# Kernel optimization log

Measured on AMD Instinct MI355X. Metric: run time of the kernel, lower is better.

Reference implementation:

```python
import jax, jax.numpy as jnp
import numpy as np

NUM_TRUE = 8
NUM_NULL = 2
NUM_EXPERTS = NUM_TRUE + NUM_NULL
TOP_K = 2


def setup_inputs() -> dict:
    key = jax.random.key(0)
    k0, k1, k2 = jax.random.split(key, 3)
    B, S, D = 4, 2048, 1024
    inputs = jax.random.normal(k0, (B, S, D), dtype=jnp.float32)
    gate_w = jax.random.normal(k1, (NUM_EXPERTS, D), dtype=jnp.float32) * 0.02
    gate_b = jnp.zeros((NUM_EXPERTS,), dtype=jnp.float32)
    # expert_w stored as [E, D_in, D_out] so expert i computes x @ expert_w[i] + expert_b[i]
    expert_w = jax.random.normal(k2, (NUM_TRUE, D, D), dtype=jnp.float32) * 0.02
    expert_b = jnp.zeros((NUM_TRUE, D), dtype=jnp.float32)
    return {"inputs": inputs, "gate_w": gate_w, "gate_b": gate_b,
            "expert_w": expert_w, "expert_b": expert_b}


def reference(inputs, gate_w, gate_b, expert_w, expert_b):
    D = inputs.shape[-1]
    x = inputs.reshape(-1, D)                       # [T, D]
    gate_logits = x @ gate_w.T + gate_b             # [T, E]
    gate_probs = jax.nn.softmax(gate_logits, axis=-1)
    weights, selected = jax.lax.top_k(gate_probs, TOP_K)  # [T, K]
    true_mask = selected < NUM_TRUE                 # null experts contribute nothing
    true_weights = weights * true_mask
    denom = true_weights.sum(axis=-1, keepdims=True)
    denom = jnp.where(denom > 0, denom, jnp.ones_like(denom))
    norm_w = (true_weights / denom).astype(x.dtype)  # [T, K]
    # per-(token, true-expert) combine weight; zero for unselected experts
    one_hot = jax.nn.one_hot(selected, NUM_EXPERTS, dtype=norm_w.dtype)  # [T, K, E]
    combine_w = jnp.einsum('tk,tke->te', norm_w, one_hot)[:, :NUM_TRUE]  # [T, E_true]
    # dense expert evaluation, then weighted combine (zero weights cancel
    # exactly as the gather/scatter loop in the torch code)
    expert_out = jnp.einsum('td,edh->teh', x, expert_w) + expert_b[None, :, :]  # [T, E_true, D]
    out = jnp.einsum('te,teh->th', combine_w, expert_out)  # [T, D]
    return out.reshape(inputs.shape[:-1] + (out.shape[-1],))
```

## Files before the change

### kernel.cpp

```cpp
#include <hip/hip_runtime.h>
#include <hip/hip_bf16.h>
#include <stdint.h>

#define T_TOKENS 8192
#define D_DIM    1024
#define NE       10
#define NT       8
#define SEG      2048

typedef unsigned short u16;
typedef __attribute__((ext_vector_type(8))) __bf16 bf16x8;
typedef __attribute__((ext_vector_type(4))) float  f32x4;
typedef __attribute__((ext_vector_type(8))) unsigned short u16x8;
typedef __attribute__((ext_vector_type(4))) unsigned short u16x4;

static __device__ __forceinline__ u16 f32_to_bf16(float f) {
  union { float f; uint32_t u; } v; v.f = f;
  uint32_t u = v.u;
  return (u16)((u + 0x7fffu + ((u >> 16) & 1u)) >> 16);
}
static __device__ __forceinline__ float bf16_to_f32(u16 u) {
  union { uint32_t u; float f; } v; v.u = ((uint32_t)u) << 16; return v.f;
}

static __device__ __forceinline__ void async_load16(const u16* g, u16* l) {
  __builtin_amdgcn_global_load_lds(
      (const __attribute__((address_space(1))) void*)(const void*)g,
      (__attribute__((address_space(3))) void*)(void*)l, 16, 0, 0);
}

union PrepShared {
  struct { float gws[NE * D_DIM]; float gbs[NE]; int se[32]; float swt[32]; } g;
  struct { float tile[64][68]; } t;
};

__global__ __launch_bounds__(256) void prep_kernel(
    const float* __restrict__ x, const float* __restrict__ gw,
    const float* __restrict__ gb, const float* __restrict__ W,
    u16* __restrict__ xb, u16* __restrict__ wT,
    int* __restrict__ cnt, int* __restrict__ tokList,
    int* __restrict__ revIdx, float* __restrict__ revW) {
  __shared__ PrepShared sh;
  int tid = threadIdx.x;

  if (blockIdx.x >= 512) {
    int tb = blockIdx.x - 512;
    int e  = tb >> 8;
    int rem = tb & 255;
    int k0 = (rem >> 4) * 64;
    int n0 = (rem & 15) * 64;
    int cr = tid & 15;
    int r0 = tid >> 4;
    const float* We = W + ((size_t)e << 20);
#pragma unroll
    for (int pass = 0; pass < 4; ++pass) {
      int r = pass * 16 + r0;
      f32x4 v = *(const f32x4*)&We[(size_t)(k0 + r) * 1024 + n0 + cr * 4];
#pragma unroll
      for (int j = 0; j < 4; ++j) sh.t.tile[cr * 4 + j][r] = v[j];
    }
    __syncthreads();
    u16* wTe = wT + ((size_t)e << 20);
#pragma unroll
    for (int pass = 0; pass < 4; ++pass) {
      int n = pass * 16 + r0;
      f32x4 tv = *(const f32x4*)&sh.t.tile[n][cr * 4];
      u16x4 pk;
#pragma unroll
      for (int j = 0; j < 4; ++j) pk[j] = f32_to_bf16(tv[j]);
      *(u16x4*)&wTe[(size_t)(n0 + n) * 1024 + k0 + cr * 4] = pk;
    }
    return;
  }

  {
    const f32x4* g4 = (const f32x4*)gw;
    f32x4* s4 = (f32x4*)sh.g.gws;
    for (int i = tid; i < NE * D_DIM / 4; i += 256) s4[i] = g4[i];
  }
  if (tid < NE) sh.g.gbs[tid] = gb[tid];
  __syncthreads();
  int lane = tid & 63;
  int wv   = tid >> 6;
  const f32x4* gws4 = (const f32x4*)sh.g.gws;
  for (int it = 0; it < 4; ++it) {
    int slot = wv * 4 + it;
    int t = blockIdx.x * 16 + slot;
    const f32x4* xr4 = (const f32x4*)(x + (size_t)t * D_DIM);
    f32x4 xv[4];
#pragma unroll
    for (int jj = 0; jj < 4; ++jj) xv[jj] = xr4[lane + 64 * jj];
    u16x4* xbr = (u16x4*)(xb + (size_t)t * D_DIM);
#pragma unroll
    for (int jj = 0; jj < 4; ++jj) {
      u16x4 pk;
#pragma unroll
      for (int k = 0; k < 4; ++k) pk[k] = f32_to_bf16(xv[jj][k]);
      xbr[lane + 64 * jj] = pk;
    }
    float logit[NE];
#pragma unroll
    for (int e = 0; e < NE; ++e) {
      float a = 0.f;
#pragma unroll
      for (int jj = 0; jj < 4; ++jj) {
        f32x4 gv = gws4[e * 256 + lane + 64 * jj];
#pragma unroll
        for (int k = 0; k < 4; ++k) a = fmaf(xv[jj][k], gv[k], a);
      }
#pragma unroll
      for (int off = 32; off >= 1; off >>= 1) a += __shfl_xor(a, off);
      logit[e] = a + sh.g.gbs[e];
    }
    float mx = logit[0];
#pragma unroll
    for (int e = 1; e < NE; ++e) mx = fmaxf(mx, logit[e]);
    float p[NE]; float s = 0.f;
#pragma unroll
    for (int e = 0; e < NE; ++e) { p[e] = expf(logit[e] - mx); s += p[e]; }
    int e0 = 0; float b0 = p[0];
#pragma unroll
    for (int e = 1; e < NE; ++e) if (p[e] > b0) { b0 = p[e]; e0 = e; }
    int e1 = -1; float b1 = -1.f;
#pragma unroll
    for (int e = 0; e < NE; ++e) if (e != e0 && p[e] > b1) { b1 = p[e]; e1 = e; }
    float w0 = b0 / s, w1 = b1 / s;
    float tw0 = (e0 < NT) ? w0 : 0.f;
    float tw1 = (e1 < NT) ? w1 : 0.f;
    float denom = tw0 + tw1;
    float nw0 = 0.f, nw1 = 0.f;
    if (denom > 0.f) { nw0 = tw0 / denom; nw1 = tw1 / denom; }
    if (lane == 0) {
      sh.g.se[slot * 2]     = (e0 < NT) ? e0 : -1;  sh.g.swt[slot * 2]     = nw0;
      sh.g.se[slot * 2 + 1] = (e1 < NT) ? e1 : -1;  sh.g.swt[slot * 2 + 1] = nw1;
      if (e0 >= NT) { revIdx[t * 2]     = -1; revW[t * 2]     = 0.f; }
      if (e1 >= NT) { revIdx[t * 2 + 1] = -1; revW[t * 2 + 1] = 0.f; }
    }
  }
  __syncthreads();
  if (tid < NT) {
    int e = tid, c = 0;
    for (int i = 0; i < 32; ++i) c += (sh.g.se[i] == e);
    if (c > 0) {
      int base = atomicAdd(&cnt[e * 32], c);
      int j = 0;
      for (int i = 0; i < 32; ++i) {
        if (sh.g.se[i] == e) {
          int tt  = blockIdx.x * 16 + (i >> 1);
          int pos = base + j;
          tokList[e * SEG + pos]   = tt;
          revIdx[tt * 2 + (i & 1)] = e * SEG + pos;
          revW[tt * 2 + (i & 1)]   = sh.g.swt[i];
          ++j;
        }
      }
    }
  }
}

__global__ __launch_bounds__(512) void moe_gemm(
    const u16* __restrict__ xb, const u16* __restrict__ wT,
    const int* __restrict__ cnt, const int* __restrict__ tokList,
    const float* __restrict__ eb, u16* __restrict__ ybuf) {
  int e  = blockIdx.x;
  int c  = cnt[e * 32];
  int m0 = blockIdx.z * 128;
  if (m0 >= c) return;
  int n0 = blockIdx.y * 128;
  __shared__ __align__(16) u16 As[3][128 * 32];
  __shared__ __align__(16) u16 Bs[3][128 * 32];
  __shared__ int tokS[128];
  int tid = threadIdx.x;
  if (tid < 128) {
    int gm = m0 + tid;
    tokS[tid] = (gm < c) ? tokList[e * SEG + gm] : tokList[e * SEG];
  }
  __syncthreads();
  int lane = tid & 63;
  int wv   = tid >> 6;
  int rl  = lane >> 2;
  int kcp = lane & 3;
  int kcd = kcp ^ ((rl >> 1) & 3);
  int rowL = wv * 16 + rl;
  const u16* gA0 = xb + (size_t)tokS[rowL] * 1024 + kcd * 8;
  const u16* wTe = wT + ((size_t)e << 20);
  const u16* gB0 = wTe + (size_t)(n0 + rowL) * 1024 + kcd * 8;
  int ldsO = (wv * 16) * 32;

  int wm = wv >> 2, wn = wv & 3;
  int lrow = lane & 15;
  int q    = lane >> 4;
  int sw   = (q ^ ((lrow >> 1) & 3)) * 8;
  f32x4 acc[4][2];
#pragma unroll
  for (int i = 0; i < 4; ++i)
#pragma unroll
    for (int j = 0; j < 2; ++j) acc[i][j] = (f32x4){0.f, 0.f, 0.f, 0.f};

#pragma unroll
  for (int p = 0; p < 2; ++p) {
    int ko = p * 32;
    async_load16(gA0 + ko, As[p] + ldsO);
    async_load16(gB0 + ko, Bs[p] + ldsO);
  }

  int cur = 0;
  for (int kt = 0; kt < 32; ++kt) {
    asm volatile("s_barrier" ::: "memory");
    if (kt < 30) {
      int st = cur - 1; if (st < 0) st += 3;
      int ko = (kt + 2) * 32;
      async_load16(gA0 + ko, As[st] + ldsO);
      async_load16(gB0 + ko, Bs[st] + ldsO);
      asm volatile("s_waitcnt vmcnt(4)" ::: "memory");
    } else if (kt == 30) {
      asm volatile("s_waitcnt vmcnt(2)" ::: "memory");
    } else {
      asm volatile("s_waitcnt vmcnt(0)" ::: "memory");
    }
    asm volatile("s_barrier" ::: "memory");
    bf16x8 af[4], bfr[2];
#pragma unroll
    for (int mt = 0; mt < 4; ++mt)
      af[mt] = *(const bf16x8*)(As[cur] + (wm * 64 + mt * 16 + lrow) * 32 + sw);
#pragma unroll
    for (int nt = 0; nt < 2; ++nt)
      bfr[nt] = *(const bf16x8*)(Bs[cur] + (wn * 32 + nt * 16 + lrow) * 32 + sw);
#pragma unroll
    for (int mt = 0; mt < 4; ++mt)
#pragma unroll
      for (int nt = 0; nt < 2; ++nt)
        acc[mt][nt] = __builtin_amdgcn_mfma_f32_16x16x32_bf16(
            af[mt], bfr[nt], acc[mt][nt], 0, 0, 0);
    ++cur; if (cur == 3) cur = 0;
  }
  int rq = lane >> 4;
  float bias[2];
#pragma unroll
  for (int nt = 0; nt < 2; ++nt)
    bias[nt] = eb[e * 1024 + n0 + wn * 32 + nt * 16 + lrow];
  u16* yb = ybuf + ((size_t)(e * SEG + m0)) * 1024 + n0 + wn * 32 + lrow;
#pragma unroll
  for (int mt = 0; mt < 4; ++mt) {
#pragma unroll
    for (int r = 0; r < 4; ++r) {
      int ml = wm * 64 + mt * 16 + rq * 4 + r;
      u16* row = yb + (size_t)ml * 1024;
#pragma unroll
      for (int nt = 0; nt < 2; ++nt)
        row[nt * 16] = f32_to_bf16(acc[mt][nt][r] + bias[nt]);
    }
  }
}

__global__ __launch_bounds__(256) void combine_kernel(
    const u16* __restrict__ ybuf, const int* __restrict__ revIdx,
    const float* __restrict__ revW, float* __restrict__ out) {
  int tid = threadIdx.x, lane = tid & 63, wv = tid >> 6;
  for (int it = 0; it < 4; ++it) {
    int t  = blockIdx.x * 16 + wv * 4 + it;
    int i0 = revIdx[t * 2], i1 = revIdx[t * 2 + 1];
    float w0 = revW[t * 2], w1 = revW[t * 2 + 1];
    float o[16];
#pragma unroll
    for (int k = 0; k < 16; ++k) o[k] = 0.f;
    if (i0 >= 0) {
      const u16x8* y = (const u16x8*)(ybuf + (size_t)i0 * 1024);
#pragma unroll
      for (int jj = 0; jj < 2; ++jj) {
        u16x8 v = y[lane + 64 * jj];
#pragma unroll
        for (int k = 0; k < 8; ++k) o[jj * 8 + k] += w0 * bf16_to_f32(v[k]);
      }
    }
    if (i1 >= 0) {
      const u16x8* y = (const u16x8*)(ybuf + (size_t)i1 * 1024);
#pragma unroll
      for (int jj = 0; jj < 2; ++jj) {
        u16x8 v = y[lane + 64 * jj];
#pragma unroll
        for (int k = 0; k < 8; ++k) o[jj * 8 + k] += w1 * bf16_to_f32(v[k]);
      }
    }
    f32x4* o4 = (f32x4*)(out + (size_t)t * 1024);
#pragma unroll
    for (int jj = 0; jj < 2; ++jj)
#pragma unroll
      for (int h = 0; h < 2; ++h) {
        f32x4 vv = {o[jj * 8 + h * 4], o[jj * 8 + h * 4 + 1],
                    o[jj * 8 + h * 4 + 2], o[jj * 8 + h * 4 + 3]};
        __builtin_nontemporal_store(vv, &o4[2 * (lane + 64 * jj) + h]);
      }
  }
}

extern "C" void kernel_launch(void* const* d_in, const int* in_sizes, int n_in,
                              void* d_out, int out_size, void* d_ws, size_t ws_size,
                              hipStream_t stream) {
  const float* x  = (const float*)d_in[0];
  const float* gw = (const float*)d_in[1];
  const float* gb = (const float*)d_in[2];
  const float* ew = (const float*)d_in[3];
  const float* eb = (const float*)d_in[4];
  float* out = (float*)d_out;
  char* ws = (char*)d_ws;
  int*   cnt     = (int*)ws;
  int*   tokList = (int*)(ws + 4096);
  int*   revIdx  = (int*)(ws + 4096 + 65536);
  float* revW    = (float*)(ws + 4096 + 131072);
  u16*   xb      = (u16*)(ws + 200704);
  u16*   wT      = (u16*)(ws + 200704 + 16777216);
  u16*   ybuf    = (u16*)(ws + 200704 + 33554432);

  hipMemsetAsync(cnt, 0, 4096, stream);
  prep_kernel<<<2560, 256, 0, stream>>>(x, gw, gb, ew, xb, wT, cnt, tokList,
                                        revIdx, revW);
  moe_gemm<<<dim3(8, 8, 16), 512, 0, stream>>>(xb, wT, cnt, tokList, eb, ybuf);
  combine_kernel<<<512, 256, 0, stream>>>(ybuf, revIdx, revW, out);
}
```

Baseline: 181.4 us.

## Enlarge MoE GEMM M-tile to 256 and spread prep/combine over more blocks

The grouped expert GEMM now computes a 256x128 output tile per block: each wave loads two A rows and issues eight M sub-tiles of MFMAs, which doubles reuse of each B fragment and halves the number of blocks along M. The wait counts are adjusted for three async loads per stage, and launch_bounds asks for 4 waves per SIMD. The prep kernel handles 8 tokens per block instead of 16, and combine handles one token per wave, so both launch more blocks. The larger tile raises register and LDS pressure and, with up to 2048 tokens per expert, leaves fewer GEMM blocks to fill the CUs.

```diff
diff --git a/kernel.cpp b/kernel.cpp
--- a/kernel.cpp
+++ b/kernel.cpp
@@ -30,7 +30,7 @@
 }
 
 union PrepShared {
-  struct { float gws[NE * D_DIM]; float gbs[NE]; int se[32]; float swt[32]; } g;
+  struct { float gws[NE * D_DIM]; float gbs[NE]; int se[16]; float swt[16]; } g;
   struct { float tile[64][68]; } t;
 };
 
@@ -43,8 +43,8 @@
   __shared__ PrepShared sh;
   int tid = threadIdx.x;
 
-  if (blockIdx.x >= 512) {
-    int tb = blockIdx.x - 512;
+  if (blockIdx.x >= 1024) {
+    int tb = blockIdx.x - 1024;
     int e  = tb >> 8;
     int rem = tb & 255;
     int k0 = (rem >> 4) * 64;
@@ -83,9 +83,9 @@
   int lane = tid & 63;
   int wv   = tid >> 6;
   const f32x4* gws4 = (const f32x4*)sh.g.gws;
-  for (int it = 0; it < 4; ++it) {
-    int slot = wv * 4 + it;
-    int t = blockIdx.x * 16 + slot;
+  for (int it = 0; it < 2; ++it) {
+    int slot = wv * 2 + it;
+    int t = blockIdx.x * 8 + slot;
     const f32x4* xr4 = (const f32x4*)(x + (size_t)t * D_DIM);
     f32x4 xv[4];
 #pragma unroll
@@ -140,13 +140,13 @@
   __syncthreads();
   if (tid < NT) {
     int e = tid, c = 0;
-    for (int i = 0; i < 32; ++i) c += (sh.g.se[i] == e);
+    for (int i = 0; i < 16; ++i) c += (sh.g.se[i] == e);
     if (c > 0) {
       int base = atomicAdd(&cnt[e * 32], c);
       int j = 0;
-      for (int i = 0; i < 32; ++i) {
+      for (int i = 0; i < 16; ++i) {
         if (sh.g.se[i] == e) {
-          int tt  = blockIdx.x * 16 + (i >> 1);
+          int tt  = blockIdx.x * 8 + (i >> 1);
           int pos = base + j;
           tokList[e * SEG + pos]   = tt;
           revIdx[tt * 2 + (i & 1)] = e * SEG + pos;
@@ -158,20 +158,20 @@
   }
 }
 
-__global__ __launch_bounds__(512) void moe_gemm(
+__global__ __launch_bounds__(512, 4) void moe_gemm(
     const u16* __restrict__ xb, const u16* __restrict__ wT,
     const int* __restrict__ cnt, const int* __restrict__ tokList,
     const float* __restrict__ eb, u16* __restrict__ ybuf) {
   int e  = blockIdx.x;
   int c  = cnt[e * 32];
-  int m0 = blockIdx.z * 128;
+  int m0 = blockIdx.z * 256;
   if (m0 >= c) return;
   int n0 = blockIdx.y * 128;
-  __shared__ __align__(16) u16 As[3][128 * 32];
+  __shared__ __align__(16) u16 As[3][256 * 32];
   __shared__ __align__(16) u16 Bs[3][128 * 32];
-  __shared__ int tokS[128];
+  __shared__ int tokS[256];
   int tid = threadIdx.x;
-  if (tid < 128) {
+  if (tid < 256) {
     int gm = m0 + tid;
     tokS[tid] = (gm < c) ? tokList[e * SEG + gm] : tokList[e * SEG];
   }
@@ -181,27 +181,30 @@
   int rl  = lane >> 2;
   int kcp = lane & 3;
   int kcd = kcp ^ ((rl >> 1) & 3);
-  int rowL = wv * 16 + rl;
-  const u16* gA0 = xb + (size_t)tokS[rowL] * 1024 + kcd * 8;
+  int rowA0 = wv * 32 + rl, rowA1 = rowA0 + 16;
+  int rowB  = wv * 16 + rl;
+  const u16* gA0 = xb + (size_t)tokS[rowA0] * 1024 + kcd * 8;
+  const u16* gA1 = xb + (size_t)tokS[rowA1] * 1024 + kcd * 8;
   const u16* wTe = wT + ((size_t)e << 20);
-  const u16* gB0 = wTe + (size_t)(n0 + rowL) * 1024 + kcd * 8;
-  int ldsO = (wv * 16) * 32;
+  const u16* gB0 = wTe + (size_t)(n0 + rowB) * 1024 + kcd * 8;
+  int ldsA0 = (wv * 32) * 32, ldsA1 = ldsA0 + 16 * 32, ldsB0 = (wv * 16) * 32;
 
   int wm = wv >> 2, wn = wv & 3;
   int lrow = lane & 15;
   int q    = lane >> 4;
   int sw   = (q ^ ((lrow >> 1) & 3)) * 8;
-  f32x4 acc[4][2];
-#pragma unroll
-  for (int i = 0; i < 4; ++i)
+  f32x4 acc[8][2];
+#pragma unroll
+  for (int i = 0; i < 8; ++i)
 #pragma unroll
     for (int j = 0; j < 2; ++j) acc[i][j] = (f32x4){0.f, 0.f, 0.f, 0.f};
 
 #pragma unroll
   for (int p = 0; p < 2; ++p) {
     int ko = p * 32;
-    async_load16(gA0 + ko, As[p] + ldsO);
-    async_load16(gB0 + ko, Bs[p] + ldsO);
+    async_load16(gA0 + ko, As[p] + ldsA0);
+    async_load16(gA1 + ko, As[p] + ldsA1);
+    async_load16(gB0 + ko, Bs[p] + ldsB0);
   }
 
   int cur = 0;
@@ -210,28 +213,28 @@
     if (kt < 30) {
       int st = cur - 1; if (st < 0) st += 3;
       int ko = (kt + 2) * 32;
-      async_load16(gA0 + ko, As[st] + ldsO);
-      async_load16(gB0 + ko, Bs[st] + ldsO);
-      asm volatile("s_waitcnt vmcnt(4)" ::: "memory");
+      async_load16(gA0 + ko, As[st] + ldsA0);
+      async_load16(gA1 + ko, As[st] + ldsA1);
+      async_load16(gB0 + ko, Bs[st] + ldsB0);
+      asm volatile("s_waitcnt vmcnt(6)" ::: "memory");
     } else if (kt == 30) {
-      asm volatile("s_waitcnt vmcnt(2)" ::: "memory");
+      asm volatile("s_waitcnt vmcnt(3)" ::: "memory");
     } else {
       asm volatile("s_waitcnt vmcnt(0)" ::: "memory");
     }
     asm volatile("s_barrier" ::: "memory");
-    bf16x8 af[4], bfr[2];
-#pragma unroll
-    for (int mt = 0; mt < 4; ++mt)
-      af[mt] = *(const bf16x8*)(As[cur] + (wm * 64 + mt * 16 + lrow) * 32 + sw);
+    bf16x8 bfr[2];
 #pragma unroll
     for (int nt = 0; nt < 2; ++nt)
       bfr[nt] = *(const bf16x8*)(Bs[cur] + (wn * 32 + nt * 16 + lrow) * 32 + sw);
 #pragma unroll
-    for (int mt = 0; mt < 4; ++mt)
+    for (int mt = 0; mt < 8; ++mt) {
+      bf16x8 af = *(const bf16x8*)(As[cur] + (wm * 128 + mt * 16 + lrow) * 32 + sw);
 #pragma unroll
       for (int nt = 0; nt < 2; ++nt)
         acc[mt][nt] = __builtin_amdgcn_mfma_f32_16x16x32_bf16(
-            af[mt], bfr[nt], acc[mt][nt], 0, 0, 0);
+            af, bfr[nt], acc[mt][nt], 0, 0, 0);
+    }
     ++cur; if (cur == 3) cur = 0;
   }
   int rq = lane >> 4;
@@ -241,10 +244,10 @@
     bias[nt] = eb[e * 1024 + n0 + wn * 32 + nt * 16 + lrow];
   u16* yb = ybuf + ((size_t)(e * SEG + m0)) * 1024 + n0 + wn * 32 + lrow;
 #pragma unroll
-  for (int mt = 0; mt < 4; ++mt) {
+  for (int mt = 0; mt < 8; ++mt) {
 #pragma unroll
     for (int r = 0; r < 4; ++r) {
-      int ml = wm * 64 + mt * 16 + rq * 4 + r;
+      int ml = wm * 128 + mt * 16 + rq * 4 + r;
       u16* row = yb + (size_t)ml * 1024;
 #pragma unroll
       for (int nt = 0; nt < 2; ++nt)
@@ -257,41 +260,39 @@
     const u16* __restrict__ ybuf, const int* __restrict__ revIdx,
     const float* __restrict__ revW, float* __restrict__ out) {
   int tid = threadIdx.x, lane = tid & 63, wv = tid >> 6;
-  for (int it = 0; it < 4; ++it) {
-    int t  = blockIdx.x * 16 + wv * 4 + it;
-    int i0 = revIdx[t * 2], i1 = revIdx[t * 2 + 1];
-    float w0 = revW[t * 2], w1 = revW[t * 2 + 1];
-    float o[16];
-#pragma unroll
-    for (int k = 0; k < 16; ++k) o[k] = 0.f;
-    if (i0 >= 0) {
-      const u16x8* y = (const u16x8*)(ybuf + (size_t)i0 * 1024);
-#pragma unroll
-      for (int jj = 0; jj < 2; ++jj) {
-        u16x8 v = y[lane + 64 * jj];
-#pragma unroll
-        for (int k = 0; k < 8; ++k) o[jj * 8 + k] += w0 * bf16_to_f32(v[k]);
-      }
-    }
-    if (i1 >= 0) {
-      const u16x8* y = (const u16x8*)(ybuf + (size_t)i1 * 1024);
-#pragma unroll
-      for (int jj = 0; jj < 2; ++jj) {
-        u16x8 v = y[lane + 64 * jj];
-#pragma unroll
-        for (int k = 0; k < 8; ++k) o[jj * 8 + k] += w1 * bf16_to_f32(v[k]);
-      }
-    }
-    f32x4* o4 = (f32x4*)(out + (size_t)t * 1024);
-#pragma unroll
-    for (int jj = 0; jj < 2; ++jj)
-#pragma unroll
-      for (int h = 0; h < 2; ++h) {
-        f32x4 vv = {o[jj * 8 + h * 4], o[jj * 8 + h * 4 + 1],
-                    o[jj * 8 + h * 4 + 2], o[jj * 8 + h * 4 + 3]};
-        __builtin_nontemporal_store(vv, &o4[2 * (lane + 64 * jj) + h]);
-      }
-  }
+  int t  = blockIdx.x * 4 + wv;
+  int i0 = revIdx[t * 2], i1 = revIdx[t * 2 + 1];
+  float w0 = revW[t * 2], w1 = revW[t * 2 + 1];
+  float o[16];
+#pragma unroll
+  for (int k = 0; k < 16; ++k) o[k] = 0.f;
+  if (i0 >= 0) {
+    const u16x8* y = (const u16x8*)(ybuf + (size_t)i0 * 1024);
+#pragma unroll
+    for (int jj = 0; jj < 2; ++jj) {
+      u16x8 v = y[lane + 64 * jj];
+#pragma unroll
+      for (int k = 0; k < 8; ++k) o[jj * 8 + k] += w0 * bf16_to_f32(v[k]);
+    }
+  }
+  if (i1 >= 0) {
+    const u16x8* y = (const u16x8*)(ybuf + (size_t)i1 * 1024);
+#pragma unroll
+    for (int jj = 0; jj < 2; ++jj) {
+      u16x8 v = y[lane + 64 * jj];
+#pragma unroll
+      for (int k = 0; k < 8; ++k) o[jj * 8 + k] += w1 * bf16_to_f32(v[k]);
+    }
+  }
+  f32x4* o4 = (f32x4*)(out + (size_t)t * 1024);
+#pragma unroll
+  for (int jj = 0; jj < 2; ++jj)
+#pragma unroll
+    for (int h = 0; h < 2; ++h) {
+      f32x4 vv = {o[jj * 8 + h * 4], o[jj * 8 + h * 4 + 1],
+                  o[jj * 8 + h * 4 + 2], o[jj * 8 + h * 4 + 3]};
+      __builtin_nontemporal_store(vv, &o4[2 * (lane + 64 * jj) + h]);
+    }
 }
 
 extern "C" void kernel_launch(void* const* d_in, const int* in_sizes, int n_in,
@@ -313,8 +314,8 @@
   u16*   ybuf    = (u16*)(ws + 200704 + 33554432);
 
   hipMemsetAsync(cnt, 0, 4096, stream);
-  prep_kernel<<<2560, 256, 0, stream>>>(x, gw, gb, ew, xb, wT, cnt, tokList,
+  prep_kernel<<<3072, 256, 0, stream>>>(x, gw, gb, ew, xb, wT, cnt, tokList,
                                         revIdx, revW);
-  moe_gemm<<<dim3(8, 8, 16), 512, 0, stream>>>(xb, wT, cnt, tokList, eb, ybuf);
-  combine_kernel<<<512, 256, 0, stream>>>(ybuf, revIdx, revW, out);
-}
+  moe_gemm<<<dim3(8, 8, 8), 512, 0, stream>>>(xb, wT, cnt, tokList, eb, ybuf);
+  combine_kernel<<<2048, 256, 0, stream>>>(ybuf, revIdx, revW, out);
+}
```

Measured after the change: 175.5 us. 3.2% less time.
